# Kernel optimization log

Hardware: AMD Instinct MI355X
Metric: run time of the kernel (lower is better)

The kernel has to match this reference:

```python
import jax, jax.numpy as jnp
import numpy as np

N_NODES = 100000
N_EDGES = 3200000
BN_EPS = 1e-5


def setup_inputs() -> dict:
    key = jax.random.key(0)
    ks = jax.random.split(key, 16)
    return {
        "x": jax.random.normal(ks[0], (N_NODES, 2), jnp.float32),
        "eq_labels": jax.random.randint(ks[1], (N_NODES,), 0, 32, jnp.int32),
        "edge_index": jax.random.randint(ks[2], (2, N_EDGES), 0, N_NODES, jnp.int32),
        "eq_emb": jax.random.normal(ks[3], (32, 8), jnp.float32),
        "W1_0": jax.random.normal(ks[4], (10, 64), jnp.float32) * 0.3,
        "b1_0": jnp.zeros((64,), jnp.float32),
        "W2_0": jax.random.normal(ks[5], (64, 64), jnp.float32) * 0.12,
        "b2_0": jnp.zeros((64,), jnp.float32),
        "eps_0": jnp.zeros((), jnp.float32),
        "gamma_0": jnp.ones((64,), jnp.float32),
        "beta_0": jnp.zeros((64,), jnp.float32),
        "W1_s": jax.random.normal(ks[6], (2, 64, 64), jnp.float32) * 0.12,
        "b1_s": jnp.zeros((2, 64), jnp.float32),
        "W2_s": jax.random.normal(ks[7], (2, 64, 64), jnp.float32) * 0.12,
        "b2_s": jnp.zeros((2, 64), jnp.float32),
        "eps_s": jnp.zeros((2,), jnp.float32),
        "gamma_s": jnp.ones((2, 64), jnp.float32),
        "beta_s": jnp.zeros((2, 64), jnp.float32),
        "Wf": jax.random.normal(ks[8], (64, 1), jnp.float32) * 0.12,
        "bf": jnp.zeros((1,), jnp.float32),
    }


def _gin_bn_relu(h, src, dst, W1, b1, W2, b2, eps, gamma, beta):
    # GINConv: (1+eps)*x_i + sum_{j->i} x_j, then 2-layer ReLU MLP, then BN, ReLU
    agg = jax.ops.segment_sum(h[src], dst, num_segments=N_NODES)
    h = (1.0 + eps) * h + agg
    h = jax.nn.relu(h @ W1 + b1)
    h = jax.nn.relu(h @ W2 + b2)
    mu = jnp.mean(h, axis=0)
    var = jnp.var(h, axis=0)
    h = (h - mu) * jax.lax.rsqrt(var + BN_EPS) * gamma + beta
    return jax.nn.relu(h)


def reference(x, eq_labels, edge_index, eq_emb, W1_0, b1_0, W2_0, b2_0, eps_0,
              gamma_0, beta_0, W1_s, b1_s, W2_s, b2_s, eps_s, gamma_s, beta_s,
              Wf, bf):
    src, dst = edge_index[0], edge_index[1]
    h = jnp.concatenate([x, eq_emb[eq_labels]], axis=-1)  # [N, 10]
    h = _gin_bn_relu(h, src, dst, W1_0, b1_0, W2_0, b2_0, eps_0, gamma_0, beta_0)
    for i in range(2):
        h = _gin_bn_relu(h, src, dst, W1_s[i], b1_s[i], W2_s[i], b2_s[i],
                         eps_s[i], gamma_s[i], beta_s[i])
    return (h @ Wf + bf).squeeze(-1)  # [N]
```

## Files before the change

### kernel.cpp

```cpp
#include <hip/hip_runtime.h>

#define N_NODES 100000
#define N_EDGES 3200000
#define BN_EPS 1e-5f

#define BLK_NODES 128
#define NBLK 782
#define CHUNK 16384
#define NW ((N_EDGES + CHUNK - 1) / CHUNK)
#define BCAP 4480
#define CUR_PAD 16
#define NSLICE 32

typedef unsigned int uint;
typedef unsigned short ushort;
typedef _Float16 half_t;
typedef __attribute__((ext_vector_type(8))) _Float16 h8v;
typedef __attribute__((ext_vector_type(4))) float f4v;

__device__ inline float bf_lo(uint u) { return __uint_as_float(u << 16); }
__device__ inline float bf_hi(uint u) { return __uint_as_float(u & 0xffff0000u); }
__device__ inline float h_lo(uint u) {
    union { ushort s; half_t h; } r; r.s = (ushort)(u & 0xffffu); return (float)r.h;
}
__device__ inline float h_hi(uint u) {
    union { ushort s; half_t h; } r; r.s = (ushort)(u >> 16); return (float)r.h;
}
__device__ inline ushort f2bf(float a) {
    uint ua = __float_as_uint(a); ua += 0x7fffu + ((ua >> 16) & 1u);
    return (ushort)(ua >> 16);
}
__device__ inline ushort f2h(float a) {
    union { half_t h; ushort u; } r;
    r.h = (half_t)a;
    return r.u;
}
__device__ inline uint packh2(float a, float b) {
    return (uint)f2h(a) | ((uint)f2h(b) << 16);
}
__device__ inline h8v loadH(const ushort* p) {
    union { uint4 q; h8v f; } r;
    r.q = *(const uint4*)p;
    return r.f;
}
__device__ inline h8v loadHh(const half_t* p) {
    union { uint4 q; h8v f; } r;
    r.q = *(const uint4*)p;
    return r.f;
}
__device__ inline f4v mfma16(h8v a, h8v b, f4v c) {
    return __builtin_amdgcn_mfma_f32_16x16x32_f16(a, b, c, 0, 0, 0);
}

__global__ __launch_bounds__(256) void k_h0(const float* __restrict__ x,
                                            const int* __restrict__ lab,
                                            const float* __restrict__ emb,
                                            float* __restrict__ h0, int n) {
    int i = blockIdx.x * blockDim.x + threadIdx.x;
    if (i >= n) return;
    float v[16];
    v[0] = x[2 * i];
    v[1] = x[2 * i + 1];
    int L = lab[i];
#pragma unroll
    for (int k = 0; k < 8; k++) v[2 + k] = emb[L * 8 + k];
#pragma unroll
    for (int k = 10; k < 16; k++) v[k] = 0.f;
    float4* o = (float4*)(h0 + (size_t)i * 16);
#pragma unroll
    for (int q = 0; q < 4; q++) {
        float4 t;
        t.x = v[4 * q]; t.y = v[4 * q + 1]; t.z = v[4 * q + 2]; t.w = v[4 * q + 3];
        o[q] = t;
    }
}

__global__ __launch_bounds__(256) void k_wcvt(const float* __restrict__ W1_0,
                                              const float* __restrict__ W2_0,
                                              const float* __restrict__ W1_s,
                                              const float* __restrict__ W2_s,
                                              ushort* __restrict__ W0t,
                                              ushort* __restrict__ W20t,
                                              ushort* __restrict__ Wst) {
    int t = threadIdx.x;
    for (int i = t; i < 64 * 32; i += 256) {
        int n = i >> 5, k = i & 31;
        W0t[i] = (k < 10) ? f2h(W1_0[k * 64 + n]) : (ushort)0;
    }
    for (int i = t; i < 4096; i += 256) {
        int n = i >> 6, k = i & 63;
        W20t[i] = f2h(W2_0[k * 64 + n]);
    }
    for (int l = 0; l < 2; l++) {
        const float* w1 = W1_s + l * 4096;
        const float* w2 = W2_s + l * 4096;
        for (int i = t; i < 4096; i += 256) {
            int n = i >> 6, k = i & 63;
            Wst[l * 8192 + i] = f2h(w1[k * 64 + n]);
            Wst[l * 8192 + 4096 + i] = f2h(w2[k * 64 + n]);
        }
    }
}

__global__ __launch_bounds__(256) void k_fill(const int* __restrict__ src,
                                              const int* __restrict__ dst,
                                              int* __restrict__ gcur,
                                              int* __restrict__ bucket) {
    __shared__ int cnt[NBLK];
    __shared__ int off[NBLK];
    int t = threadIdx.x;
    for (int b = t; b < NBLK; b += 256) cnt[b] = 0;
    __syncthreads();
    int my0 = blockIdx.x * CHUNK + t * 64;
    for (int k = 0; k < 64; k += 4) {
        int e = my0 + k;
        if (e + 3 < N_EDGES) {
            int4 d4 = *(const int4*)(dst + e);
            atomicAdd(&cnt[d4.x >> 7], 1);
            atomicAdd(&cnt[d4.y >> 7], 1);
            atomicAdd(&cnt[d4.z >> 7], 1);
            atomicAdd(&cnt[d4.w >> 7], 1);
        } else {
#pragma unroll
            for (int kk = 0; kk < 4; kk++) {
                int ee = e + kk;
                if (ee < N_EDGES) atomicAdd(&cnt[dst[ee] >> 7], 1);
            }
        }
    }
    __syncthreads();
    for (int b = t; b < NBLK; b += 256) {
        int c = cnt[b];
        off[b] = (c > 0) ? atomicAdd(&gcur[b * CUR_PAD], c) : 0;
    }
    __syncthreads();
    for (int k = 0; k < 64; k += 4) {
        int e = my0 + k;
        if (e + 3 < N_EDGES) {
            int4 d4 = *(const int4*)(dst + e);
            int4 s4 = *(const int4*)(src + e);
            int dd[4] = {d4.x, d4.y, d4.z, d4.w};
            int ss[4] = {s4.x, s4.y, s4.z, s4.w};
#pragma unroll
            for (int kk = 0; kk < 4; kk++) {
                int b = dd[kk] >> 7;
                int p = atomicAdd(&off[b], 1);
                if (p < BCAP)
                    bucket[(size_t)b * BCAP + p] = ((dd[kk] & 127) << 17) | ss[kk];
            }
        } else {
#pragma unroll
            for (int kk = 0; kk < 4; kk++) {
                int ee = e + kk;
                if (ee < N_EDGES) {
                    int d = dst[ee], s = src[ee];
                    int b = d >> 7;
                    int p = atomicAdd(&off[b], 1);
                    if (p < BCAP)
                        bucket[(size_t)b * BCAP + p] = ((d & 127) << 17) | s;
                }
            }
        }
    }
}

__global__ __launch_bounds__(256) void k_sort(const int* __restrict__ gcur,
                                              const int* __restrict__ bucket,
                                              int* __restrict__ col2,
                                              int2* __restrict__ nodeoff, int n) {
    __shared__ int cnt[BLK_NODES];
    __shared__ int scn[BLK_NODES];
    __shared__ int cur[BLK_NODES];
    int t = threadIdx.x;
    int blk = blockIdx.x;
    if (t < BLK_NODES) cnt[t] = 0;
    __syncthreads();
    int cc = min(gcur[blk * CUR_PAD], BCAP);
    const int* bb = bucket + (size_t)blk * BCAP;
    for (int i = t; i < cc; i += 256) atomicAdd(&cnt[bb[i] >> 17], 1);
    __syncthreads();
    if (t < BLK_NODES) scn[t] = cnt[t];
    __syncthreads();
#pragma unroll
    for (int off = 1; off < BLK_NODES; off <<= 1) {
        int v = (t >= off && t < BLK_NODES) ? scn[t - off] : 0;
        __syncthreads();
        if (t < BLK_NODES) scn[t] += v;
        __syncthreads();
    }
    if (t < BLK_NODES) {
        int start = scn[t] - cnt[t];
        cur[t] = start;
        int node = blk * BLK_NODES + t;
        if (node < n) nodeoff[node] = int2{blk * BCAP + start, cnt[t]};
    }
    __syncthreads();
    int* out = col2 + (size_t)blk * BCAP;
    for (int i = t; i < cc; i += 256) {
        int w = bb[i];
        int p = atomicAdd(&cur[w >> 17], 1);
        out[p] = w & 0x1FFFF;
    }
}

__global__ __launch_bounds__(256, 4) void k_layer0M(const float* __restrict__ h0,
                                                    const int2* __restrict__ nodeoff,
                                                    const int* __restrict__ col,
                                                    const float* __restrict__ epsp,
                                                    const ushort* __restrict__ W0t,
                                                    const float* __restrict__ b1,
                                                    const ushort* __restrict__ W20t,
                                                    const float* __restrict__ b2,
                                                    ushort* __restrict__ hraw,
                                                    float* __restrict__ part_out) {
    __shared__ half_t buf[4][16][72];
    int t = threadIdx.x, w = t >> 6, lane = t & 63;
    int base = blockIdx.x * 64 + w * 16;
    float ep = 1.f + *epsp;
    int hl = lane >> 5, l5 = lane & 31;
    int q = l5 & 3, g = l5 >> 2;
    const float4* h4 = (const float4*)h0;

    int nj = base + (lane & 15);
    int2 no2 = nodeoff[nj];
    int myStart = no2.x;
    int myDeg = (nj < N_NODES) ? no2.y : 0;

    int stC, dgC, mxC, wvC, wv2C;
    {
        stC = __shfl(myStart, hl, 64);
        dgC = __shfl(myDeg, hl, 64);
        int dA = __shfl(myDeg, 0, 64), dB = __shfl(myDeg, 1, 64);
        mxC = max(dA, dB);
        wvC = (dgC > 0) ? col[stC + min(l5, dgC - 1)] : 0;
        wv2C = (mxC > 32) ? ((dgC > 32) ? col[stC + min(32 + l5, dgC - 1)] : wvC) : 0;
    }

    for (int r = 0; r < 8; r++) {
        int stN = 0, dgN = 0, mxN = 0, wvN = 0, wv2N = 0;
        if (r < 7) {
            stN = __shfl(myStart, 2 * (r + 1) + hl, 64);
            dgN = __shfl(myDeg, 2 * (r + 1) + hl, 64);
            int dA = __shfl(myDeg, 2 * (r + 1), 64);
            int dB = __shfl(myDeg, 2 * (r + 1) + 1, 64);
            mxN = max(dA, dB);
            wvN = (dgN > 0) ? col[stN + min(l5, dgN - 1)] : 0;
            wv2N = (mxN > 32) ? ((dgN > 32) ? col[stN + min(32 + l5, dgN - 1)] : wvN) : 0;
        }
        int deg = dgC, mx = mxC;
        float ac[4] = {0.f, 0.f, 0.f, 0.f};
        if (mx > 0) {
            int idx[4];
#pragma unroll
            for (int i = 0; i < 4; i++) idx[i] = __shfl(wvC, (hl << 5) + g + 8 * i, 64);
            float4 rows[4];
#pragma unroll
            for (int i = 0; i < 4; i++) rows[i] = h4[(size_t)idx[i] * 4 + q];
#pragma unroll
            for (int i = 0; i < 4; i++) {
                float m = (g + 8 * i < deg) ? 1.f : 0.f;
                ac[0] = fmaf(m, rows[i].x, ac[0]);
                ac[1] = fmaf(m, rows[i].y, ac[1]);
                ac[2] = fmaf(m, rows[i].z, ac[2]);
                ac[3] = fmaf(m, rows[i].w, ac[3]);
            }
            if (mx > 32) {
                int idx2[4];
#pragma unroll
                for (int i = 0; i < 4; i++) idx2[i] = __shfl(wv2C, (hl << 5) + g + 8 * i, 64);
                float4 rows2[4];
#pragma unroll
                for (int i = 0; i < 4; i++) rows2[i] = h4[(size_t)idx2[i] * 4 + q];
#pragma unroll
                for (int i = 0; i < 4; i++) {
                    float m = (32 + g + 8 * i < deg) ? 1.f : 0.f;
                    ac[0] = fmaf(m, rows2[i].x, ac[0]);
                    ac[1] = fmaf(m, rows2[i].y, ac[1]);
                    ac[2] = fmaf(m, rows2[i].z, ac[2]);
                    ac[3] = fmaf(m, rows2[i].w, ac[3]);
                }
                for (int e = 64 + g; e < deg; e += 8) {
                    float4 v = h4[(size_t)col[stC + e] * 4 + q];
                    ac[0] += v.x; ac[1] += v.y; ac[2] += v.z; ac[3] += v.w;
                }
            }
        }
#pragma unroll
        for (int o = 4; o < 32; o <<= 1) {
#pragma unroll
            for (int k = 0; k < 4; k++) ac[k] += __shfl_xor(ac[k], o, 64);
        }
        int node = base + 2 * r + hl;
        bool valid = node < N_NODES;
        int nodeC = valid ? node : 0;
        float vm = valid ? ep : 0.f;
        float4 xi = h4[(size_t)nodeC * 4 + q];
        ac[0] = fmaf(vm, xi.x, ac[0]);
        ac[1] = fmaf(vm, xi.y, ac[1]);
        ac[2] = fmaf(vm, xi.z, ac[2]);
        ac[3] = fmaf(vm, xi.w, ac[3]);
        if (!valid) { ac[0] = ac[1] = ac[2] = ac[3] = 0.f; }
        if (g == 0) {
            int nl = 2 * r + hl;
            *(uint2*)&buf[w][nl][q * 4] = uint2{packh2(ac[0], ac[1]), packh2(ac[2], ac[3])};
            *(uint2*)&buf[w][nl][16 + q * 4] = uint2{0u, 0u};
        }
        stC = stN; dgC = dgN; mxC = mxN; wvC = wvN; wv2C = wv2N;
    }
    int mr = lane & 15, kq = lane >> 4, nc = lane & 15;
    h8v A0 = loadHh(&buf[w][mr][kq * 8]);
#pragma unroll
    for (int nt = 0; nt < 4; nt++) {
        float bb = b1[nt * 16 + nc];
        f4v c = {bb, bb, bb, bb};
        c = mfma16(A0, loadH(W0t + (nt * 16 + nc) * 32 + kq * 8), c);
#pragma unroll
        for (int r2 = 0; r2 < 4; r2++)
            buf[w][kq * 4 + r2][nt * 16 + nc] = (half_t)fmaxf(c[r2], 0.f);
    }
    h8v P0 = loadHh(&buf[w][mr][kq * 8]);
    h8v P1 = loadHh(&buf[w][mr][32 + kq * 8]);
    float sA[4], sB[4];
#pragma unroll
    for (int nt = 0; nt < 4; nt++) { sA[nt] = 0.f; sB[nt] = 0.f; }
#pragma unroll
    for (int nt = 0; nt < 4; nt++) {
        float bb = b2[nt * 16 + nc];
        f4v c = {bb, bb, bb, bb};
        c = mfma16(P0, loadH(W20t + (nt * 16 + nc) * 64 + kq * 8), c);
        c = mfma16(P1, loadH(W20t + (nt * 16 + nc) * 64 + 32 + kq * 8), c);
#pragma unroll
        for (int r2 = 0; r2 < 4; r2++) {
            int node = base + kq * 4 + r2;
            float vv = fmaxf(c[r2], 0.f);
            if (node < N_NODES) {
                sA[nt] += vv;
                sB[nt] = fmaf(vv, vv, sB[nt]);
                hraw[(size_t)node * 64 + nt * 16 + nc] = f2h(vv);
            }
        }
    }
#pragma unroll
    for (int o = 16; o < 64; o <<= 1) {
#pragma unroll
        for (int nt = 0; nt < 4; nt++) {
            sA[nt] += __shfl_xor(sA[nt], o, 64);
            sB[nt] += __shfl_xor(sB[nt], o, 64);
        }
    }
    if (kq == 0) {
        float* pp = part_out + (blockIdx.x & (NSLICE - 1)) * 128;
#pragma unroll
        for (int nt = 0; nt < 4; nt++) {
            atomicAdd(&pp[nt * 16 + nc], sA[nt]);
            atomicAdd(&pp[64 + nt * 16 + nc], sB[nt]);
        }
    }
}

__global__ __launch_bounds__(256) void k_act(const ushort* __restrict__ hraw,
                                             const float* __restrict__ part,
                                             const float* __restrict__ gamma,
                                             const float* __restrict__ beta,
                                             ushort* __restrict__ act, float invn) {
    __shared__ float st[128];
    __shared__ float sc[64], sh[64];
    int t = threadIdx.x;
    if (t < 128) {
        float S = 0.f;
#pragma unroll 8
        for (int s = 0; s < NSLICE; s++) S += part[s * 128 + t];
        st[t] = S;
    }
    __syncthreads();
    if (t < 64) {
        float mu = st[t] * invn;
        float var = fmaxf(st[64 + t] * invn - mu * mu, 0.f);
        float s = gamma[t] * rsqrtf(var + BN_EPS);
        sc[t] = s;
        sh[t] = beta[t] - mu * s;
    }
    __syncthreads();
    int base = (blockIdx.x * 256 + t) * 4;
    int f0 = base & 63;
    uint2 hv = *(const uint2*)(hraw + base);
    float a0 = fmaxf(fmaf(h_lo(hv.x), sc[f0 + 0], sh[f0 + 0]), 0.f);
    float a1 = fmaxf(fmaf(h_hi(hv.x), sc[f0 + 1], sh[f0 + 1]), 0.f);
    float a2 = fmaxf(fmaf(h_lo(hv.y), sc[f0 + 2], sh[f0 + 2]), 0.f);
    float a3 = fmaxf(fmaf(h_hi(hv.y), sc[f0 + 3], sh[f0 + 3]), 0.f);
    uint2 o;
    o.x = (uint)f2bf(a0) | ((uint)f2bf(a1) << 16);
    o.y = (uint)f2bf(a2) | ((uint)f2bf(a3) << 16);
    *(uint2*)(act + base) = o;
}

__global__ __launch_bounds__(256, 4) void k_layerM(const uint* __restrict__ actin,
                                                   const int2* __restrict__ nodeoff,
                                                   const int* __restrict__ col,
                                                   const float* __restrict__ epsp,
                                                   const ushort* __restrict__ W1t,
                                                   const float* __restrict__ b1,
                                                   const ushort* __restrict__ W2t,
                                                   const float* __restrict__ b2,
                                                   ushort* __restrict__ hraw,
                                                   float* __restrict__ part_out) {
    __shared__ half_t buf[4][16][72];
    int t = threadIdx.x, w = t >> 6, lane = t & 63;
    int base = blockIdx.x * 64 + w * 16;
    float ep = 1.f + *epsp;
    int hl = lane >> 5, l5 = lane & 31;
    int q = l5 & 7, g = l5 >> 3;
    const uint4* hb4 = (const uint4*)actin;

    int nj = base + (lane & 15);
    int2 no2 = nodeoff[nj];
    int myStart = no2.x;
    int myDeg = (nj < N_NODES) ? no2.y : 0;

    int stC, dgC, mxC, wvC, wv2C;
    {
        stC = __shfl(myStart, hl, 64);
        dgC = __shfl(myDeg, hl, 64);
        int dA = __shfl(myDeg, 0, 64), dB = __shfl(myDeg, 1, 64);
        mxC = max(dA, dB);
        wvC = (dgC > 0) ? col[stC + min(l5, dgC - 1)] : 0;
        wv2C = (mxC > 32) ? ((dgC > 32) ? col[stC + min(32 + l5, dgC - 1)] : wvC) : 0;
    }

    for (int r = 0; r < 8; r++) {
        int stN = 0, dgN = 0, mxN = 0, wvN = 0, wv2N = 0;
        if (r < 7) {
            stN = __shfl(myStart, 2 * (r + 1) + hl, 64);
            dgN = __shfl(myDeg, 2 * (r + 1) + hl, 64);
            int dA = __shfl(myDeg, 2 * (r + 1), 64);
            int dB = __shfl(myDeg, 2 * (r + 1) + 1, 64);
            mxN = max(dA, dB);
            wvN = (dgN > 0) ? col[stN + min(l5, dgN - 1)] : 0;
            wv2N = (mxN > 32) ? ((dgN > 32) ? col[stN + min(32 + l5, dgN - 1)] : wvN) : 0;
        }
        int deg = dgC, mx = mxC;
        float acc[8];
#pragma unroll
        for (int k = 0; k < 8; k++) acc[k] = 0.f;
        auto procm = [&](uint4 v, float m) {
            acc[0] = fmaf(m, bf_lo(v.x), acc[0]);
            acc[1] = fmaf(m, bf_hi(v.x), acc[1]);
            acc[2] = fmaf(m, bf_lo(v.y), acc[2]);
            acc[3] = fmaf(m, bf_hi(v.y), acc[3]);
            acc[4] = fmaf(m, bf_lo(v.z), acc[4]);
            acc[5] = fmaf(m, bf_hi(v.z), acc[5]);
            acc[6] = fmaf(m, bf_lo(v.w), acc[6]);
            acc[7] = fmaf(m, bf_hi(v.w), acc[7]);
        };
        if (mx > 0) {
            int idx[8];
#pragma unroll
            for (int i = 0; i < 8; i++) idx[i] = __shfl(wvC, (hl << 5) + g + 4 * i, 64);
            uint4 rows[8];
#pragma unroll
            for (int i = 0; i < 8; i++) rows[i] = hb4[(size_t)idx[i] * 8 + q];
#pragma unroll
            for (int i = 0; i < 8; i++) procm(rows[i], (g + 4 * i < deg) ? 1.f : 0.f);
            if (mx > 32) {
                int idx2[8];
#pragma unroll
                for (int i = 0; i < 8; i++) idx2[i] = __shfl(wv2C, (hl << 5) + g + 4 * i, 64);
                uint4 rows2[8];
#pragma unroll
                for (int i = 0; i < 8; i++) rows2[i] = hb4[(size_t)idx2[i] * 8 + q];
#pragma unroll
                for (int i = 0; i < 8; i++) procm(rows2[i], (32 + g + 4 * i < deg) ? 1.f : 0.f);
                for (int e = 64 + g; e < deg; e += 4)
                    procm(hb4[(size_t)col[stC + e] * 8 + q], 1.f);
            }
        }
#pragma unroll
        for (int o = 8; o < 32; o <<= 1) {
#pragma unroll
            for (int k = 0; k < 8; k++) acc[k] += __shfl_xor(acc[k], o, 64);
        }
        int node = base + 2 * r + hl;
        bool valid = node < N_NODES;
        int nodeC = valid ? node : 0;
        float vm = valid ? ep : 0.f;
        uint4 v = hb4[(size_t)nodeC * 8 + q];
        acc[0] = fmaf(vm, bf_lo(v.x), acc[0]);
        acc[1] = fmaf(vm, bf_hi(v.x), acc[1]);
        acc[2] = fmaf(vm, bf_lo(v.y), acc[2]);
        acc[3] = fmaf(vm, bf_hi(v.y), acc[3]);
        acc[4] = fmaf(vm, bf_lo(v.z), acc[4]);
        acc[5] = fmaf(vm, bf_hi(v.z), acc[5]);
        acc[6] = fmaf(vm, bf_lo(v.w), acc[6]);
        acc[7] = fmaf(vm, bf_hi(v.w), acc[7]);
        if (!valid) {
#pragma unroll
            for (int k = 0; k < 8; k++) acc[k] = 0.f;
        }
        if (g == 0) {
            int nl = 2 * r + hl;
            *(uint2*)&buf[w][nl][q * 8 + 0] = uint2{packh2(acc[0], acc[1]), packh2(acc[2], acc[3])};
            *(uint2*)&buf[w][nl][q * 8 + 4] = uint2{packh2(acc[4], acc[5]), packh2(acc[6], acc[7])};
        }
        stC = stN; dgC = dgN; mxC = mxN; wvC = wvN; wv2C = wv2N;
    }
    int mr = lane & 15, kq = lane >> 4, nc = lane & 15;
    h8v A0 = loadHh(&buf[w][mr][kq * 8]);
    h8v A1 = loadHh(&buf[w][mr][32 + kq * 8]);
#pragma unroll
    for (int nt = 0; nt < 4; nt++) {
        float bb = b1[nt * 16 + nc];
        f4v c = {bb, bb, bb, bb};
        c = mfma16(A0, loadH(W1t + (nt * 16 + nc) * 64 + kq * 8), c);
        c = mfma16(A1, loadH(W1t + (nt * 16 + nc) * 64 + 32 + kq * 8), c);
#pragma unroll
        for (int r2 = 0; r2 < 4; r2++)
            buf[w][kq * 4 + r2][nt * 16 + nc] = (half_t)fmaxf(c[r2], 0.f);
    }
    h8v P0 = loadHh(&buf[w][mr][kq * 8]);
    h8v P1 = loadHh(&buf[w][mr][32 + kq * 8]);
    float sA[4], sB[4];
#pragma unroll
    for (int nt = 0; nt < 4; nt++) { sA[nt] = 0.f; sB[nt] = 0.f; }
#pragma unroll
    for (int nt = 0; nt < 4; nt++) {
        float bb = b2[nt * 16 + nc];
        f4v c = {bb, bb, bb, bb};
        c = mfma16(P0, loadH(W2t + (nt * 16 + nc) * 64 + kq * 8), c);
        c = mfma16(P1, loadH(W2t + (nt * 16 + nc) * 64 + 32 + kq * 8), c);
#pragma unroll
        for (int r2 = 0; r2 < 4; r2++) {
            int node = base + kq * 4 + r2;
            float vv = fmaxf(c[r2], 0.f);
            if (node < N_NODES) {
                sA[nt] += vv;
                sB[nt] = fmaf(vv, vv, sB[nt]);
                hraw[(size_t)node * 64 + nt * 16 + nc] = f2h(vv);
            }
        }
    }
#pragma unroll
    for (int o = 16; o < 64; o <<= 1) {
#pragma unroll
        for (int nt = 0; nt < 4; nt++) {
            sA[nt] += __shfl_xor(sA[nt], o, 64);
            sB[nt] += __shfl_xor(sB[nt], o, 64);
        }
    }
    if (kq == 0) {
        float* pp = part_out + (blockIdx.x & (NSLICE - 1)) * 128;
#pragma unroll
        for (int nt = 0; nt < 4; nt++) {
            atomicAdd(&pp[nt * 16 + nc], sA[nt]);
            atomicAdd(&pp[64 + nt * 16 + nc], sB[nt]);
        }
    }
}

__global__ __launch_bounds__(256) void k_out(const ushort* __restrict__ hraw,
                                             const float* __restrict__ part,
                                             const float* __restrict__ gamma,
                                             const float* __restrict__ beta,
                                             const float* __restrict__ Wf,
                                             const float* __restrict__ bfp,
                                             float* __restrict__ out, int n,
                                             float invn) {
    __shared__ float st[128];
    __shared__ float sc[64], sh[64];
    int t = threadIdx.x;
    if (t < 128) {
        float S = 0.f;
#pragma unroll 8
        for (int s = 0; s < NSLICE; s++) S += part[s * 128 + t];
        st[t] = S;
    }
    __syncthreads();
    if (t < 64) {
        float mu = st[t] * invn;
        float var = fmaxf(st[64 + t] * invn - mu * mu, 0.f);
        float s = gamma[t] * rsqrtf(var + BN_EPS);
        sc[t] = s;
        sh[t] = beta[t] - mu * s;
    }
    __syncthreads();
    int i = blockIdx.x * blockDim.x + threadIdx.x;
    if (i >= n) return;
    float acc = *bfp;
    const uint2* h2 = (const uint2*)(hraw + (size_t)i * 64);
#pragma unroll
    for (int qq = 0; qq < 16; qq++) {
        uint2 v = h2[qq];
        int j = qq * 4;
        acc = fmaf(fmaxf(fmaf(h_lo(v.x), sc[j + 0], sh[j + 0]), 0.f), Wf[j + 0], acc);
        acc = fmaf(fmaxf(fmaf(h_hi(v.x), sc[j + 1], sh[j + 1]), 0.f), Wf[j + 1], acc);
        acc = fmaf(fmaxf(fmaf(h_lo(v.y), sc[j + 2], sh[j + 2]), 0.f), Wf[j + 2], acc);
        acc = fmaf(fmaxf(fmaf(h_hi(v.y), sc[j + 3], sh[j + 3]), 0.f), Wf[j + 3], acc);
    }
    out[i] = acc;
}

extern "C" void kernel_launch(void* const* d_in, const int* in_sizes, int n_in,
                              void* d_out, int out_size, void* d_ws, size_t ws_size,
                              hipStream_t stream) {
    const float* x      = (const float*)d_in[0];
    const int*   lab    = (const int*)d_in[1];
    const int*   edge   = (const int*)d_in[2];
    const float* emb    = (const float*)d_in[3];
    const float* W1_0   = (const float*)d_in[4];
    const float* b1_0   = (const float*)d_in[5];
    const float* W2_0   = (const float*)d_in[6];
    const float* b2_0   = (const float*)d_in[7];
    const float* eps_0  = (const float*)d_in[8];
    const float* gamma_0= (const float*)d_in[9];
    const float* beta_0 = (const float*)d_in[10];
    const float* W1_s   = (const float*)d_in[11];
    const float* b1_s   = (const float*)d_in[12];
    const float* W2_s   = (const float*)d_in[13];
    const float* b2_s   = (const float*)d_in[14];
    const float* eps_s  = (const float*)d_in[15];
    const float* gamma_s= (const float*)d_in[16];
    const float* beta_s = (const float*)d_in[17];
    const float* Wf     = (const float*)d_in[18];
    const float* bf     = (const float*)d_in[19];

    const int N = N_NODES, E = N_EDGES;
    const int* srcp = edge;
    const int* dstp = edge + E;

    char* p = (char*)d_ws;
    auto alloc = [&](size_t bytes) {
        void* r = (void*)p;
        p += (bytes + 255) & ~(size_t)255;
        return r;
    };
    int* bucket  = (int*)alloc((size_t)NBLK * BCAP * 4);
    int* col2    = (int*)alloc((size_t)NBLK * BCAP * 4);
    int* gcur    = (int*)alloc((size_t)NBLK * CUR_PAD * 4);
    int* nodeoff = (int*)alloc((size_t)(N + 64) * 8);
    ushort* hraw = (ushort*)alloc((size_t)N * 64 * 2);
    ushort* act  = (ushort*)alloc((size_t)N * 64 * 2);
    float* h0    = (float*)alloc((size_t)N * 16 * 4);
    float* parts = (float*)alloc(3 * NSLICE * 128 * 4);
    ushort* W0t  = (ushort*)alloc(64 * 32 * 2);
    ushort* W20t = (ushort*)alloc(4096 * 2);
    ushort* Wst  = (ushort*)alloc(2 * 8192 * 2);

    hipMemsetAsync(gcur, 0, (size_t)NBLK * CUR_PAD * 4, stream);
    hipMemsetAsync(parts, 0, 3 * NSLICE * 128 * 4, stream);

    const int TB = 256;
    const int gN = (N + TB - 1) / TB;
    const int gM = (N + 63) / 64;
    const int gA = N * 64 / 1024;
    const float invn = 1.0f / (float)N;

    k_h0<<<gN, TB, 0, stream>>>(x, lab, emb, h0, N);
    k_wcvt<<<1, TB, 0, stream>>>(W1_0, W2_0, W1_s, W2_s, W0t, W20t, Wst);
    k_fill<<<NW, TB, 0, stream>>>(srcp, dstp, gcur, bucket);
    k_sort<<<NBLK, TB, 0, stream>>>(gcur, bucket, col2, (int2*)nodeoff, N);

    k_layer0M<<<gM, TB, 0, stream>>>(h0, (const int2*)nodeoff, col2, eps_0, W0t,
                                     b1_0, W20t, b2_0, hraw,
                                     parts + 0 * NSLICE * 128);
    k_act<<<gA, TB, 0, stream>>>(hraw, parts + 0 * NSLICE * 128, gamma_0, beta_0,
                                 act, invn);

    k_layerM<<<gM, TB, 0, stream>>>((const uint*)act, (const int2*)nodeoff, col2,
                                    eps_s + 0, Wst + 0 * 8192, b1_s + 0 * 64,
                                    Wst + 0 * 8192 + 4096, b2_s + 0 * 64,
                                    hraw, parts + 1 * NSLICE * 128);
    k_act<<<gA, TB, 0, stream>>>(hraw, parts + 1 * NSLICE * 128, gamma_s + 0 * 64,
                                 beta_s + 0 * 64, act, invn);

    k_layerM<<<gM, TB, 0, stream>>>((const uint*)act, (const int2*)nodeoff, col2,
                                    eps_s + 1, Wst + 1 * 8192, b1_s + 1 * 64,
                                    Wst + 1 * 8192 + 4096, b2_s + 1 * 64,
                                    hraw, parts + 2 * NSLICE * 128);

    k_out<<<gN, TB, 0, stream>>>(hraw, parts + 2 * NSLICE * 128,
                                 gamma_s + 1 * 64, beta_s + 1 * 64, Wf, bf,
                                 (float*)d_out, N, invn);
}
```

Baseline: 394.8 us.

## Store layer-0 input features as fp16 and fold weight conversion into k_h0

The 16-wide layer-0 node features are now stored as fp16 instead of fp32, which halves the bytes fetched by the 3.2M-edge gather in layer 0. The aggregation unpacks the fp16 values to fp32 before accumulating. The separate weight-conversion kernel is merged into k_h0, with block 0 doing the conversion, which removes one launch. The cost is reduced precision on the raw input features and some extra unpack instructions in the gather loop.

```diff
diff --git a/kernel.cpp b/kernel.cpp
--- a/kernel.cpp
+++ b/kernel.cpp
@@ -55,49 +55,49 @@
 __global__ __launch_bounds__(256) void k_h0(const float* __restrict__ x,
                                             const int* __restrict__ lab,
                                             const float* __restrict__ emb,
-                                            float* __restrict__ h0, int n) {
+                                            ushort* __restrict__ h0,
+                                            const float* __restrict__ W1_0,
+                                            const float* __restrict__ W2_0,
+                                            const float* __restrict__ W1_s,
+                                            const float* __restrict__ W2_s,
+                                            ushort* __restrict__ W0t,
+                                            ushort* __restrict__ W20t,
+                                            ushort* __restrict__ Wst, int n) {
     int i = blockIdx.x * blockDim.x + threadIdx.x;
-    if (i >= n) return;
-    float v[16];
-    v[0] = x[2 * i];
-    v[1] = x[2 * i + 1];
-    int L = lab[i];
-#pragma unroll
-    for (int k = 0; k < 8; k++) v[2 + k] = emb[L * 8 + k];
-#pragma unroll
-    for (int k = 10; k < 16; k++) v[k] = 0.f;
-    float4* o = (float4*)(h0 + (size_t)i * 16);
-#pragma unroll
-    for (int q = 0; q < 4; q++) {
-        float4 t;
-        t.x = v[4 * q]; t.y = v[4 * q + 1]; t.z = v[4 * q + 2]; t.w = v[4 * q + 3];
-        o[q] = t;
-    }
-}
-
-__global__ __launch_bounds__(256) void k_wcvt(const float* __restrict__ W1_0,
-                                              const float* __restrict__ W2_0,
-                                              const float* __restrict__ W1_s,
-                                              const float* __restrict__ W2_s,
-                                              ushort* __restrict__ W0t,
-                                              ushort* __restrict__ W20t,
-                                              ushort* __restrict__ Wst) {
-    int t = threadIdx.x;
-    for (int i = t; i < 64 * 32; i += 256) {
-        int n = i >> 5, k = i & 31;
-        W0t[i] = (k < 10) ? f2h(W1_0[k * 64 + n]) : (ushort)0;
-    }
-    for (int i = t; i < 4096; i += 256) {
-        int n = i >> 6, k = i & 63;
-        W20t[i] = f2h(W2_0[k * 64 + n]);
-    }
-    for (int l = 0; l < 2; l++) {
-        const float* w1 = W1_s + l * 4096;
-        const float* w2 = W2_s + l * 4096;
-        for (int i = t; i < 4096; i += 256) {
-            int n = i >> 6, k = i & 63;
-            Wst[l * 8192 + i] = f2h(w1[k * 64 + n]);
-            Wst[l * 8192 + 4096 + i] = f2h(w2[k * 64 + n]);
+    if (i < n) {
+        float v[16];
+        v[0] = x[2 * i];
+        v[1] = x[2 * i + 1];
+        int L = lab[i];
+#pragma unroll
+        for (int k = 0; k < 8; k++) v[2 + k] = emb[L * 8 + k];
+#pragma unroll
+        for (int k = 10; k < 16; k++) v[k] = 0.f;
+        uint o8[8];
+#pragma unroll
+        for (int k = 0; k < 8; k++) o8[k] = packh2(v[2 * k], v[2 * k + 1]);
+        uint4* o = (uint4*)(h0 + (size_t)i * 16);
+        o[0] = uint4{o8[0], o8[1], o8[2], o8[3]};
+        o[1] = uint4{o8[4], o8[5], o8[6], o8[7]};
+    }
+    if (blockIdx.x == 0) {
+        int t = threadIdx.x;
+        for (int j = t; j < 64 * 32; j += 256) {
+            int nn = j >> 5, k = j & 31;
+            W0t[j] = (k < 10) ? f2h(W1_0[k * 64 + nn]) : (ushort)0;
+        }
+        for (int j = t; j < 4096; j += 256) {
+            int nn = j >> 6, k = j & 63;
+            W20t[j] = f2h(W2_0[k * 64 + nn]);
+        }
+        for (int l = 0; l < 2; l++) {
+            const float* w1 = W1_s + l * 4096;
+            const float* w2 = W2_s + l * 4096;
+            for (int j = t; j < 4096; j += 256) {
+                int nn = j >> 6, k = j & 63;
+                Wst[l * 8192 + j] = f2h(w1[k * 64 + nn]);
+                Wst[l * 8192 + 4096 + j] = f2h(w2[k * 64 + nn]);
+            }
         }
     }
 }
@@ -203,7 +203,7 @@
     }
 }
 
-__global__ __launch_bounds__(256, 4) void k_layer0M(const float* __restrict__ h0,
+__global__ __launch_bounds__(256, 4) void k_layer0M(const ushort* __restrict__ h0,
                                                     const int2* __restrict__ nodeoff,
                                                     const int* __restrict__ col,
                                                     const float* __restrict__ epsp,
@@ -219,7 +219,7 @@
     float ep = 1.f + *epsp;
     int hl = lane >> 5, l5 = lane & 31;
     int q = l5 & 3, g = l5 >> 2;
-    const float4* h4 = (const float4*)h0;
+    const uint* hb = (const uint*)h0;
 
     int nj = base + (lane & 15);
     int2 no2 = nodeoff[nj];
@@ -253,35 +253,38 @@
             int idx[4];
 #pragma unroll
             for (int i = 0; i < 4; i++) idx[i] = __shfl(wvC, (hl << 5) + g + 8 * i, 64);
-            float4 rows[4];
-#pragma unroll
-            for (int i = 0; i < 4; i++) rows[i] = h4[(size_t)idx[i] * 4 + q];
+            uint2 rows[4];
+#pragma unroll
+            for (int i = 0; i < 4; i++)
+                rows[i] = *(const uint2*)(hb + (size_t)idx[i] * 8 + q * 2);
 #pragma unroll
             for (int i = 0; i < 4; i++) {
                 float m = (g + 8 * i < deg) ? 1.f : 0.f;
-                ac[0] = fmaf(m, rows[i].x, ac[0]);
-                ac[1] = fmaf(m, rows[i].y, ac[1]);
-                ac[2] = fmaf(m, rows[i].z, ac[2]);
-                ac[3] = fmaf(m, rows[i].w, ac[3]);
+                ac[0] = fmaf(m, h_lo(rows[i].x), ac[0]);
+                ac[1] = fmaf(m, h_hi(rows[i].x), ac[1]);
+                ac[2] = fmaf(m, h_lo(rows[i].y), ac[2]);
+                ac[3] = fmaf(m, h_hi(rows[i].y), ac[3]);
             }
             if (mx > 32) {
                 int idx2[4];
 #pragma unroll
                 for (int i = 0; i < 4; i++) idx2[i] = __shfl(wv2C, (hl << 5) + g + 8 * i, 64);
-                float4 rows2[4];
-#pragma unroll
-                for (int i = 0; i < 4; i++) rows2[i] = h4[(size_t)idx2[i] * 4 + q];
+                uint2 rows2[4];
+#pragma unroll
+                for (int i = 0; i < 4; i++)
+                    rows2[i] = *(const uint2*)(hb + (size_t)idx2[i] * 8 + q * 2);
 #pragma unroll
                 for (int i = 0; i < 4; i++) {
                     float m = (32 + g + 8 * i < deg) ? 1.f : 0.f;
-                    ac[0] = fmaf(m, rows2[i].x, ac[0]);
-                    ac[1] = fmaf(m, rows2[i].y, ac[1]);
-                    ac[2] = fmaf(m, rows2[i].z, ac[2]);
-                    ac[3] = fmaf(m, rows2[i].w, ac[3]);
+                    ac[0] = fmaf(m, h_lo(rows2[i].x), ac[0]);
+                    ac[1] = fmaf(m, h_hi(rows2[i].x), ac[1]);
+                    ac[2] = fmaf(m, h_lo(rows2[i].y), ac[2]);
+                    ac[3] = fmaf(m, h_hi(rows2[i].y), ac[3]);
                 }
                 for (int e = 64 + g; e < deg; e += 8) {
-                    float4 v = h4[(size_t)col[stC + e] * 4 + q];
-                    ac[0] += v.x; ac[1] += v.y; ac[2] += v.z; ac[3] += v.w;
+                    uint2 v = *(const uint2*)(hb + (size_t)col[stC + e] * 8 + q * 2);
+                    ac[0] += h_lo(v.x); ac[1] += h_hi(v.x);
+                    ac[2] += h_lo(v.y); ac[3] += h_hi(v.y);
                 }
             }
         }
@@ -294,11 +297,11 @@
         bool valid = node < N_NODES;
         int nodeC = valid ? node : 0;
         float vm = valid ? ep : 0.f;
-        float4 xi = h4[(size_t)nodeC * 4 + q];
-        ac[0] = fmaf(vm, xi.x, ac[0]);
-        ac[1] = fmaf(vm, xi.y, ac[1]);
-        ac[2] = fmaf(vm, xi.z, ac[2]);
-        ac[3] = fmaf(vm, xi.w, ac[3]);
+        uint2 sv = *(const uint2*)(hb + (size_t)nodeC * 8 + q * 2);
+        ac[0] = fmaf(vm, h_lo(sv.x), ac[0]);
+        ac[1] = fmaf(vm, h_hi(sv.x), ac[1]);
+        ac[2] = fmaf(vm, h_lo(sv.y), ac[2]);
+        ac[3] = fmaf(vm, h_hi(sv.y), ac[3]);
         if (!valid) { ac[0] = ac[1] = ac[2] = ac[3] = 0.f; }
         if (g == 0) {
             int nl = 2 * r + hl;
@@ -638,7 +641,7 @@
     int* nodeoff = (int*)alloc((size_t)(N + 64) * 8);
     ushort* hraw = (ushort*)alloc((size_t)N * 64 * 2);
     ushort* act  = (ushort*)alloc((size_t)N * 64 * 2);
-    float* h0    = (float*)alloc((size_t)N * 16 * 4);
+    ushort* h0   = (ushort*)alloc((size_t)N * 16 * 2);
     float* parts = (float*)alloc(3 * NSLICE * 128 * 4);
     ushort* W0t  = (ushort*)alloc(64 * 32 * 2);
     ushort* W20t = (ushort*)alloc(4096 * 2);
@@ -653,8 +656,8 @@
     const int gA = N * 64 / 1024;
     const float invn = 1.0f / (float)N;
 
-    k_h0<<<gN, TB, 0, stream>>>(x, lab, emb, h0, N);
-    k_wcvt<<<1, TB, 0, stream>>>(W1_0, W2_0, W1_s, W2_s, W0t, W20t, Wst);
+    k_h0<<<gN, TB, 0, stream>>>(x, lab, emb, h0, W1_0, W2_0, W1_s, W2_s,
+                                W0t, W20t, Wst, N);
     k_fill<<<NW, TB, 0, stream>>>(srcp, dstp, gcur, bucket);
     k_sort<<<NBLK, TB, 0, stream>>>(gcur, bucket, col2, (int2*)nodeoff, N);
 
```

Measured after the change: 392.1 us. No clear change (-0.7%).
